# Kernel optimization log

Hardware: AMD Instinct MI355X
Metric: run time of the kernel (lower is better)

## Reference

```python
import jax, jax.numpy as jnp
import numpy as np

H = 512  # hidden_size


def setup_inputs() -> dict:
    key = jax.random.key(0)
    k1, k2, k3, k4, k5, k6 = jax.random.split(key, 6)
    B, S = 32, 2048
    output = jax.random.normal(k1, (B, H), dtype=jnp.float32)
    encoder_outputs = jax.random.normal(k2, (B, S, 2 * H), dtype=jnp.float32)
    encoder_mask = jax.random.randint(k3, (B, S), 0, 2, dtype=jnp.int32)
    # nn.Linear(3H, H): weight [H, 3H], bias [H]
    bound = 1.0 / np.sqrt(3 * H)
    W_attn = jax.random.uniform(k4, (H, 3 * H), minval=-bound, maxval=bound, dtype=jnp.float32)
    b_attn = jax.random.uniform(k5, (H,), minval=-bound, maxval=bound, dtype=jnp.float32)
    v = jax.random.normal(k6, (H,), dtype=jnp.float32) * (1.0 / np.sqrt(H))
    return {"output": output, "encoder_outputs": encoder_outputs,
            "encoder_mask": encoder_mask, "W_attn": W_attn, "b_attn": b_attn, "v": v}


def reference(output, encoder_outputs, encoder_mask, W_attn, b_attn, v):
    # Equivalent to cat([repeat(output), enc], -1) @ W.T: split W into state/enc blocks
    W_s = W_attn[:, :H]        # [H, H]   acts on decoder state
    W_e = W_attn[:, H:]        # [H, 2H]  acts on encoder outputs
    state_proj = output @ W_s.T                              # [B, H]
    enc_proj = jnp.einsum('bse,he->bsh', encoder_outputs, W_e)  # [B, S, H]
    energy = jnp.tanh(state_proj[:, None, :] + enc_proj + b_attn)  # [B, S, H]
    scores = jnp.einsum('bsh,h->bs', energy, v)[:, None, :]   # [B, 1, S]
    scores = scores - 1000.0 * (encoder_mask[:, None, :] == 0).astype(scores.dtype)
    return jax.nn.softmax(scores, axis=2)
```

## Files before the change

kernel.cpp:

```cpp
#include <hip/hip_runtime.h>
#include <hip/hip_bf16.h>

typedef __attribute__((ext_vector_type(4))) float f32x4;
typedef __attribute__((ext_vector_type(8))) short short8;

#define HH 512
#define BB 32
#define SS 2048
#define KK 1024

__device__ __forceinline__ unsigned short f2bf(float f) {
    unsigned int u = __float_as_uint(f);
    u += 0x7fffu + ((u >> 16) & 1u);
    return (unsigned short)(u >> 16);
}

__device__ __forceinline__ ushort4 pack4(float4 f) {
    ushort4 p;
    p.x = f2bf(f.x); p.y = f2bf(f.y); p.z = f2bf(f.z); p.w = f2bf(f.w);
    return p;
}

__device__ __forceinline__ float fast_tanh(float x) {
    float e = __expf(2.0f * x);
    return 1.0f - 2.0f / (e + 1.0f);
}

__device__ __forceinline__ void dma16(const float* g, float* l) {
    __builtin_amdgcn_global_load_lds(
        (__attribute__((address_space(1))) const void*)g,
        (__attribute__((address_space(3))) void*)l, 16, 0, 0);
}

#define FENCE() asm volatile("" ::: "memory")

__device__ __forceinline__ short8 cvt_bf8(f32x4 a0, f32x4 a1) {
    short8 o;
    #pragma unroll
    for (int i = 0; i < 4; ++i) {
        union { __hip_bfloat16 h; unsigned short u; } c0, c1;
        c0.h = __float2bfloat16(a0[i]);
        c1.h = __float2bfloat16(a1[i]);
        o[i]     = (short)c0.u;
        o[i + 4] = (short)c1.u;
    }
    return o;
}

__global__ __launch_bounds__(256)
void spb_kernel(const float* __restrict__ out_state,
                const float* __restrict__ W,
                const float* __restrict__ bias,
                float* __restrict__ spb) {
    int wave = threadIdx.x >> 6, lane = threadIdx.x & 63;
    int g = blockIdx.x * 4 + wave;
    int b = g >> 9, h = g & 511;
    const float* wr = W + (size_t)h * 1536;
    const float* ov = out_state + b * HH;
    float4 w0 = *(const float4*)(wr + lane * 8);
    float4 w1 = *(const float4*)(wr + lane * 8 + 4);
    float4 o0 = *(const float4*)(ov + lane * 8);
    float4 o1 = *(const float4*)(ov + lane * 8 + 4);
    float d = w0.x * o0.x + w0.y * o0.y + w0.z * o0.z + w0.w * o0.w
            + w1.x * o1.x + w1.y * o1.y + w1.z * o1.z + w1.w * o1.w;
    d += __shfl_xor(d, 1); d += __shfl_xor(d, 2); d += __shfl_xor(d, 4);
    d += __shfl_xor(d, 8); d += __shfl_xor(d, 16); d += __shfl_xor(d, 32);
    if (lane == 0) spb[g] = d + bias[h];
}

__global__ void wconv_kernel(const float* __restrict__ W, unsigned short* __restrict__ Wt) {
    int idx = blockIdx.x * 256 + threadIdx.x;
    int e8 = idx * 8;
    int h = e8 >> 10;
    int k = e8 & 1023;
    const float* src = W + (size_t)h * 1536 + 512 + k;
    float4 w0 = *(const float4*)src;
    float4 w1 = *(const float4*)(src + 4);
    int kt = k >> 5;
    int q  = (k >> 3) & 3;
    int g  = h >> 4;
    int r  = h & 15;
    int ln = (q << 4) | r;
    unsigned short* dst = Wt + (size_t)kt * 16384 + g * 512 + ln * 8;
    *(ushort4*)dst = pack4(w0);
    *(ushort4*)(dst + 4) = pack4(w1);
}

__global__ __launch_bounds__(512, 2)
void attn_gemm(const float* __restrict__ enc, const unsigned short* __restrict__ Wt,
               const float* __restrict__ spb, const float* __restrict__ vvec,
               float* __restrict__ scores) {
    __shared__ __align__(16) float Asm[2][16384];

    const int tid = threadIdx.x;
    const int w = tid >> 6;
    const int lane = tid & 63;
    const int r = lane & 15;
    const int q = lane >> 4;
    const int b = blockIdx.x >> 4;
    const int s0 = (blockIdx.x & 15) << 7;
    const int bS = b * SS + s0;

    const int l32 = lane & 31, lhi = lane >> 5;
    const int rowA = w * 4 + lhi;
    const int rowB = w * 4 + 2 + lhi;
    const float* aP0 = enc + (size_t)(bS + rowA) * KK + ((l32 ^ (rowA & 7)) << 2);
    const float* aP1 = enc + (size_t)(bS + rowB) * KK + ((l32 ^ (rowB & 7)) << 2);
    const int ad0 = (w * 4) * 128 + lane * 4;
    const int ad1 = (w * 4 + 2) * 128 + lane * 4;

    const short8* wp = (const short8*)(Wt + (size_t)(w * 4) * 512 + lane * 8);

    const int ark = r & 7;
    const int qb = q * 2;
    const int arf = r * 128;

    f32x4 acc[8][4] = {};
    short8 bfr[2][4];

    #pragma unroll
    for (int s = 0; s < 4; ++s) {
        dma16(aP0 + (size_t)s * 32 * KK, &Asm[0][s * 32 * 128 + ad0]);
        dma16(aP1 + (size_t)s * 32 * KK, &Asm[0][s * 32 * 128 + ad1]);
    }
    FENCE();
    #pragma unroll
    for (int nf = 0; nf < 4; ++nf) bfr[0][nf] = wp[nf * 64];
    FENCE();
    asm volatile("s_waitcnt vmcnt(4) lgkmcnt(0)" ::: "memory");
    __builtin_amdgcn_s_barrier();
    __builtin_amdgcn_sched_barrier(0);

    for (int e = 0; e < 7; ++e) {
        const float* abase = &Asm[e & 1][0];
        float* sdst = &Asm[(e & 1) ^ 1][0];
        const size_t koff = (size_t)(e + 1) * 128;
        #pragma unroll
        for (int s = 0; s < 4; ++s) {
            const int ktn = e * 4 + s + 1;
            if (s < 3) {
                #pragma unroll
                for (int nf = 0; nf < 4; ++nf)
                    bfr[(s + 1) & 1][nf] = wp[(size_t)ktn * 2048 + nf * 64];
                FENCE();
                dma16(aP0 + koff + (size_t)s * 32 * KK, sdst + s * 32 * 128 + ad0);
                dma16(aP1 + koff + (size_t)s * 32 * KK, sdst + s * 32 * 128 + ad1);
                FENCE();
            } else {
                dma16(aP0 + koff + (size_t)3 * 32 * KK, sdst + 3 * 32 * 128 + ad0);
                dma16(aP1 + koff + (size_t)3 * 32 * KK, sdst + 3 * 32 * 128 + ad1);
                FENCE();
                #pragma unroll
                for (int nf = 0; nf < 4; ++nf)
                    bfr[0][nf] = wp[(size_t)ktn * 2048 + nf * 64];
                FENCE();
            }
            const int u0 = ((s * 8 + qb) ^ ark) << 2;
            const int u1 = ((s * 8 + qb + 1) ^ ark) << 2;
            #pragma unroll
            for (int mt = 0; mt < 8; ++mt) {
                const int rowf = mt * 2048 + arf;
                f32x4 a0 = *(const f32x4*)(abase + rowf + u0);
                f32x4 a1 = *(const f32x4*)(abase + rowf + u1);
                short8 af = cvt_bf8(a0, a1);
                #pragma unroll
                for (int nf = 0; nf < 4; ++nf)
                    acc[mt][nf] = __builtin_amdgcn_mfma_f32_16x16x32_bf16(
                        af, bfr[s & 1][nf], acc[mt][nf], 0, 0, 0);
            }
        }
        asm volatile("s_waitcnt vmcnt(4) lgkmcnt(0)" ::: "memory");
        __builtin_amdgcn_s_barrier();
        __builtin_amdgcn_sched_barrier(0);
    }

    {
        const float* abase = &Asm[1][0];
        #pragma unroll
        for (int s = 0; s < 4; ++s) {
            if (s < 3) {
                const int ktn = 29 + s;
                #pragma unroll
                for (int nf = 0; nf < 4; ++nf)
                    bfr[(s + 1) & 1][nf] = wp[(size_t)ktn * 2048 + nf * 64];
                FENCE();
            }
            const int u0 = ((s * 8 + qb) ^ ark) << 2;
            const int u1 = ((s * 8 + qb + 1) ^ ark) << 2;
            #pragma unroll
            for (int mt = 0; mt < 8; ++mt) {
                const int rowf = mt * 2048 + arf;
                f32x4 a0 = *(const f32x4*)(abase + rowf + u0);
                f32x4 a1 = *(const f32x4*)(abase + rowf + u1);
                short8 af = cvt_bf8(a0, a1);
                #pragma unroll
                for (int nf = 0; nf < 4; ++nf)
                    acc[mt][nf] = __builtin_amdgcn_mfma_f32_16x16x32_bf16(
                        af, bfr[s & 1][nf], acc[mt][nf], 0, 0, 0);
            }
        }
    }

    float* red = (float*)&Asm[0][0];
    float vh[4], sh[4];
    #pragma unroll
    for (int nf = 0; nf < 4; ++nf) {
        int h = w * 64 + nf * 16 + r;
        vh[nf] = vvec[h];
        sh[nf] = spb[b * HH + h];
    }
    float rowacc[8][4] = {};
    #pragma unroll
    for (int mt = 0; mt < 8; ++mt)
        #pragma unroll
        for (int nf = 0; nf < 4; ++nf)
            #pragma unroll
            for (int i = 0; i < 4; ++i) {
                float x = acc[mt][nf][i] + sh[nf];
                rowacc[mt][i] += vh[nf] * fast_tanh(x);
            }
    #pragma unroll
    for (int mt = 0; mt < 8; ++mt)
        #pragma unroll
        for (int i = 0; i < 4; ++i) {
            float t = rowacc[mt][i];
            t += __shfl_xor(t, 1);
            t += __shfl_xor(t, 2);
            t += __shfl_xor(t, 4);
            t += __shfl_xor(t, 8);
            rowacc[mt][i] = t;
        }
    if (r == 0) {
        #pragma unroll
        for (int mt = 0; mt < 8; ++mt)
            #pragma unroll
            for (int i = 0; i < 4; ++i)
                red[w * 128 + mt * 16 + q * 4 + i] = rowacc[mt][i];
    }
    __syncthreads();
    if (tid < 128) {
        float sum = 0.f;
        #pragma unroll
        for (int ww = 0; ww < 8; ++ww) sum += red[ww * 128 + tid];
        scores[bS + tid] = sum;
    }
}

__global__ void softmax_kernel(const float* __restrict__ scores,
                               const int* __restrict__ mask,
                               float* __restrict__ out) {
    __shared__ float red[256];
    int b = blockIdx.x, tid = threadIdx.x;
    float x[8];
    #pragma unroll
    for (int i = 0; i < 8; ++i) {
        int s = tid + i * 256;
        float sc = scores[b * SS + s];
        if (mask[b * SS + s] == 0) sc -= 1000.0f;
        x[i] = sc;
    }
    float mx = x[0];
    #pragma unroll
    for (int i = 1; i < 8; ++i) mx = fmaxf(mx, x[i]);
    red[tid] = mx;
    __syncthreads();
    for (int o = 128; o > 0; o >>= 1) {
        if (tid < o) red[tid] = fmaxf(red[tid], red[tid + o]);
        __syncthreads();
    }
    mx = red[0];
    __syncthreads();
    float e[8], sum = 0.f;
    #pragma unroll
    for (int i = 0; i < 8; ++i) { e[i] = __expf(x[i] - mx); sum += e[i]; }
    red[tid] = sum;
    __syncthreads();
    for (int o = 128; o > 0; o >>= 1) {
        if (tid < o) red[tid] += red[tid + o];
        __syncthreads();
    }
    float inv = 1.0f / red[0];
    #pragma unroll
    for (int i = 0; i < 8; ++i) out[b * SS + tid + i * 256] = e[i] * inv;
}

extern "C" void kernel_launch(void* const* d_in, const int* in_sizes, int n_in,
                              void* d_out, int out_size, void* d_ws, size_t ws_size,
                              hipStream_t stream) {
    const float* out_state = (const float*)d_in[0];
    const float* enc       = (const float*)d_in[1];
    const int*   mask      = (const int*)d_in[2];
    const float* W_attn    = (const float*)d_in[3];
    const float* b_attn    = (const float*)d_in[4];
    const float* vvec      = (const float*)d_in[5];
    float* out = (float*)d_out;

    char* ws = (char*)d_ws;
    float*          spb    = (float*)ws;
    unsigned short* Wt     = (unsigned short*)(ws + 65536);
    float*          scores = (float*)(ws + 65536 + 1048576);

    spb_kernel<<<4096, 256, 0, stream>>>(out_state, W_attn, b_attn, spb);
    wconv_kernel<<<256, 256, 0, stream>>>(W_attn, Wt);
    attn_gemm<<<512, 512, 0, stream>>>(enc, Wt, spb, vvec, scores);
    softmax_kernel<<<32, 256, 0, stream>>>(scores, mask, out);
}
```

Baseline: 413.1 us.

## Load all four W fragments per stage up front instead of double-buffered prefetch

Replaces the fine-grained interleaving of per-substep W-fragment prefetch and A-tile DMA with a bulk load of all 16 W fragments at the start of each K-stage, followed by issuing all A DMAs, then the MFMA loop. Waits now drain vmcnt fully (vmcnt(0)) before each barrier. A syncthreads is added before the reduction writes to shared memory. The aim is a simpler schedule with fewer waits per substep, at the cost of more registers and exposing the W load latency at the start of each stage.

```diff
diff --git a/kernel.cpp b/kernel.cpp
--- a/kernel.cpp
+++ b/kernel.cpp
@@ -116,7 +116,6 @@
     const int arf = r * 128;
 
     f32x4 acc[8][4] = {};
-    short8 bfr[2][4];
 
     #pragma unroll
     for (int s = 0; s < 4; ++s) {
@@ -124,10 +123,7 @@
         dma16(aP1 + (size_t)s * 32 * KK, &Asm[0][s * 32 * 128 + ad1]);
     }
     FENCE();
-    #pragma unroll
-    for (int nf = 0; nf < 4; ++nf) bfr[0][nf] = wp[nf * 64];
-    FENCE();
-    asm volatile("s_waitcnt vmcnt(4) lgkmcnt(0)" ::: "memory");
+    asm volatile("s_waitcnt vmcnt(0)" ::: "memory");
     __builtin_amdgcn_s_barrier();
     __builtin_amdgcn_sched_barrier(0);
 
@@ -135,26 +131,22 @@
         const float* abase = &Asm[e & 1][0];
         float* sdst = &Asm[(e & 1) ^ 1][0];
         const size_t koff = (size_t)(e + 1) * 128;
+
+        short8 bfr[4][4];
+        #pragma unroll
+        for (int kt2 = 0; kt2 < 4; ++kt2)
+            #pragma unroll
+            for (int nf = 0; nf < 4; ++nf)
+                bfr[kt2][nf] = wp[(size_t)(e * 4 + kt2) * 2048 + nf * 64];
+        FENCE();
         #pragma unroll
         for (int s = 0; s < 4; ++s) {
-            const int ktn = e * 4 + s + 1;
-            if (s < 3) {
-                #pragma unroll
-                for (int nf = 0; nf < 4; ++nf)
-                    bfr[(s + 1) & 1][nf] = wp[(size_t)ktn * 2048 + nf * 64];
-                FENCE();
-                dma16(aP0 + koff + (size_t)s * 32 * KK, sdst + s * 32 * 128 + ad0);
-                dma16(aP1 + koff + (size_t)s * 32 * KK, sdst + s * 32 * 128 + ad1);
-                FENCE();
-            } else {
-                dma16(aP0 + koff + (size_t)3 * 32 * KK, sdst + 3 * 32 * 128 + ad0);
-                dma16(aP1 + koff + (size_t)3 * 32 * KK, sdst + 3 * 32 * 128 + ad1);
-                FENCE();
-                #pragma unroll
-                for (int nf = 0; nf < 4; ++nf)
-                    bfr[0][nf] = wp[(size_t)ktn * 2048 + nf * 64];
-                FENCE();
-            }
+            dma16(aP0 + koff + (size_t)s * 32 * KK, sdst + s * 32 * 128 + ad0);
+            dma16(aP1 + koff + (size_t)s * 32 * KK, sdst + s * 32 * 128 + ad1);
+        }
+        FENCE();
+        #pragma unroll
+        for (int s = 0; s < 4; ++s) {
             const int u0 = ((s * 8 + qb) ^ ark) << 2;
             const int u1 = ((s * 8 + qb + 1) ^ ark) << 2;
             #pragma unroll
@@ -166,25 +158,25 @@
                 #pragma unroll
                 for (int nf = 0; nf < 4; ++nf)
                     acc[mt][nf] = __builtin_amdgcn_mfma_f32_16x16x32_bf16(
-                        af, bfr[s & 1][nf], acc[mt][nf], 0, 0, 0);
+                        af, bfr[s][nf], acc[mt][nf], 0, 0, 0);
             }
         }
-        asm volatile("s_waitcnt vmcnt(4) lgkmcnt(0)" ::: "memory");
+        asm volatile("s_waitcnt vmcnt(0) lgkmcnt(0)" ::: "memory");
         __builtin_amdgcn_s_barrier();
         __builtin_amdgcn_sched_barrier(0);
     }
 
     {
         const float* abase = &Asm[1][0];
+        short8 bfr[4][4];
+        #pragma unroll
+        for (int kt2 = 0; kt2 < 4; ++kt2)
+            #pragma unroll
+            for (int nf = 0; nf < 4; ++nf)
+                bfr[kt2][nf] = wp[(size_t)(28 + kt2) * 2048 + nf * 64];
+        FENCE();
         #pragma unroll
         for (int s = 0; s < 4; ++s) {
-            if (s < 3) {
-                const int ktn = 29 + s;
-                #pragma unroll
-                for (int nf = 0; nf < 4; ++nf)
-                    bfr[(s + 1) & 1][nf] = wp[(size_t)ktn * 2048 + nf * 64];
-                FENCE();
-            }
             const int u0 = ((s * 8 + qb) ^ ark) << 2;
             const int u1 = ((s * 8 + qb + 1) ^ ark) << 2;
             #pragma unroll
@@ -196,7 +188,7 @@
                 #pragma unroll
                 for (int nf = 0; nf < 4; ++nf)
                     acc[mt][nf] = __builtin_amdgcn_mfma_f32_16x16x32_bf16(
-                        af, bfr[s & 1][nf], acc[mt][nf], 0, 0, 0);
+                        af, bfr[s][nf], acc[mt][nf], 0, 0, 0);
             }
         }
     }
@@ -230,6 +222,7 @@
             t += __shfl_xor(t, 8);
             rowacc[mt][i] = t;
         }
+    __syncthreads();
     if (r == 0) {
         #pragma unroll
         for (int mt = 0; mt < 8; ++mt)
```

Result: no change. 413.3 us (+0.1%).
